# Performance work log

Measured on AMD Instinct MI355X. Metric: run time of the kernel, lower is better.

## Reference

```python
import jax, jax.numpy as jnp
import numpy as np

F_IN, U, N_CLS = 256, 512, 50


def _gru_scan(x_tbf, W, Uk, b):
    """Keras GRU (reset_after=True, tanh/sigmoid). x_tbf: [T,B,F]. Returns [T,B,U]."""
    b_in, b_rec = b[0], b[1]                 # each [3U]
    xg = jnp.einsum('tbf,fg->tbg', x_tbf, W) + b_in   # precompute input gates [T,B,3U]
    B = x_tbf.shape[1]
    h0 = jnp.zeros((B, U), dtype=x_tbf.dtype)

    def step(h, xt):
        rec = h @ Uk + b_rec                 # [B,3U]
        xz, xr, xh = jnp.split(xt, 3, axis=-1)
        rz, rr, rh = jnp.split(rec, 3, axis=-1)
        z = jax.nn.sigmoid(xz + rz)
        r = jax.nn.sigmoid(xr + rr)
        hh = jnp.tanh(xh + r * rh)
        h_new = z * h + (1.0 - z) * hh
        return h_new, h_new

    _, ys = jax.lax.scan(step, h0, xg)
    return ys


def setup_inputs() -> dict:
    key = jax.random.key(0)
    ks = jax.random.split(key, 10)
    x = jax.random.normal(ks[0], (32, 1024, F_IN), dtype=jnp.float32)
    # glorot-ish scales
    s_w = (2.0 / (F_IN + 3 * U)) ** 0.5
    s_u = (2.0 / (U + 3 * U)) ** 0.5
    s_d = (2.0 / (2 * U + N_CLS)) ** 0.5
    Wf = jax.random.normal(ks[1], (F_IN, 3 * U), dtype=jnp.float32) * s_w
    Uf = jax.random.normal(ks[2], (U, 3 * U), dtype=jnp.float32) * s_u
    bf = jnp.zeros((2, 3 * U), dtype=jnp.float32)
    Wb = jax.random.normal(ks[3], (F_IN, 3 * U), dtype=jnp.float32) * s_w
    Ub = jax.random.normal(ks[4], (U, 3 * U), dtype=jnp.float32) * s_u
    bb = jnp.zeros((2, 3 * U), dtype=jnp.float32)
    Wd = jax.random.normal(ks[5], (2 * U, N_CLS), dtype=jnp.float32) * s_d
    bd = jnp.zeros((N_CLS,), dtype=jnp.float32)
    return {"x": x, "Wf": Wf, "Uf": Uf, "bf": bf, "Wb": Wb, "Ub": Ub, "bb": bb, "Wd": Wd, "bd": bd}


def reference(x, Wf, Uf, bf, Wb, Ub, bb, Wd, bd):
    # training=False -> dropout / recurrent_dropout are identity.
    x_tbf = jnp.transpose(x, (1, 0, 2))                       # [T,B,F]
    fwd = _gru_scan(x_tbf, Wf, Uf, bf)                        # [T,B,U]
    bwd = _gru_scan(x_tbf[::-1], Wb, Ub, bb)[::-1]            # reversed-in, re-reversed out
    h = jnp.concatenate([fwd, bwd], axis=-1)                  # [T,B,2U]
    h = jnp.transpose(h, (1, 0, 2))                           # [B,T,2U]
    logits = jnp.einsum('btd,dc->btc', h, Wd) + bd            # [B,T,50]
    return jax.nn.softmax(logits, axis=-1)
```

## Files before the change

kernel.cpp:

```cpp
#include <hip/hip_runtime.h>
#include <hip/hip_bf16.h>

#define F_IN  256
#define UNITS 512
#define T_SEQ 1024
#define B_SZ  32
#define NCLS  50
#define NG    16
#define NWAVE 6
#define NTAGS 96
#define SCOPE __HIP_MEMORY_SCOPE_AGENT

typedef short s16x8 __attribute__((ext_vector_type(8)));
typedef float f32x16 __attribute__((ext_vector_type(16)));

__device__ __forceinline__ ushort f2bf(float f) {
  union { float f; unsigned u; } v; v.f = f;
  unsigned r = v.u + 0x7fffu + ((v.u >> 16) & 1u);
  return (ushort)(r >> 16);
}


__global__ void prep_xT(const float* __restrict__ x, ushort* __restrict__ xT) {
  int idx = blockIdx.x * 256 + threadIdx.x;
  int b = idx >> 15;
  int r = idx & 32767;
  int t = r >> 5;
  int c = r & 31;
  const float4* s4 = (const float4*)(x + ((size_t)b * T_SEQ + t) * F_IN + c * 8);
  float4 f0 = s4[0], f1 = s4[1];
  s16x8 o;
  o[0] = (short)f2bf(f0.x); o[1] = (short)f2bf(f0.y);
  o[2] = (short)f2bf(f0.z); o[3] = (short)f2bf(f0.w);
  o[4] = (short)f2bf(f1.x); o[5] = (short)f2bf(f1.y);
  o[6] = (short)f2bf(f1.z); o[7] = (short)f2bf(f1.w);
  *(s16x8*)(xT + ((size_t)t * B_SZ + b) * F_IN + c * 8) = o;
}

__global__ void prep_UWT(const float* __restrict__ Uf, const float* __restrict__ Wf,
                         const float* __restrict__ Ub, const float* __restrict__ Wb,
                         ushort* __restrict__ UWT) {
  int idx = blockIdx.x * 256 + threadIdx.x;
  int d = idx / 147456;
  int r = idx % 147456;
  int n = r / 96;
  int ck = r % 96;
  const float* U = d ? Ub : Uf;
  const float* W = d ? Wb : Wf;
  s16x8 o;
  #pragma unroll
  for (int i = 0; i < 8; ++i) {
    int k = ck * 8 + i;
    float v = (k < UNITS) ? U[(size_t)k * 1536 + n] : W[(size_t)(k - UNITS) * 1536 + n];
    o[i] = (short)f2bf(v);
  }
  *(s16x8*)(UWT + ((size_t)d * 1536 + n) * 768 + ck * 8) = o;
}

__global__ void prep_WdT(const float* __restrict__ Wd, ushort* __restrict__ WdT) {
  int idx = blockIdx.x * 256 + threadIdx.x;
  int n = idx >> 10, k = idx & 1023;
  float v = (n < NCLS) ? Wd[(size_t)k * NCLS + n] : 0.f;
  WdT[idx] = f2bf(v);
}

__global__ __launch_bounds__(384, 2) void gru_rec(
    const ushort* __restrict__ xT,
    const ushort* __restrict__ UWT,
    const float* __restrict__ bias_f,
    const float* __restrict__ bias_b,
    ushort* __restrict__ h_out,
    unsigned* __restrict__ tags)
{
  const int g  = blockIdx.x;
  const int d  = g >> 4;
  const int gg = g & 15;
  const int tid  = threadIdx.x;
  const int wv   = tid >> 6;
  const int lane = tid & 63;
  const int col  = lane & 31;
  const int half = lane >> 5;
  const int gate = wv >> 1;
  const int kh   = wv & 1;

  __shared__ float slot[2][32][128];

  s16x8 bfrag[24];
  {
    const ushort* bp = UWT + ((size_t)d * 1536 + gate * UNITS + gg * 32 + col) * 768
                       + kh * 384 + half * 8;
    #pragma unroll
    for (int c = 0; c < 24; ++c) bfrag[c] = *(const s16x8*)(bp + c * 16);
  }

  const float* bias = d ? bias_b : bias_f;
  float bz[3], br[3], bih[3], brh[3], hprev[3];
  #pragma unroll
  for (int i = 0; i < 3; ++i) {
    int e = tid + 384 * i;
    int j = gg * 32 + (e & 31);
    bz[i] = br[i] = bih[i] = brh[i] = 0.f;
    hprev[i] = 0.f;
    if (e < 1024) {
      bz[i]  = bias[j]        + bias[1536 + j];
      br[i]  = bias[512 + j]  + bias[1536 + 512 + j];
      bih[i] = bias[1024 + j];
      brh[i] = bias[1536 + 1024 + j];
    }
  }

  for (int s = 0; s < T_SEQ; ++s) {
    const int t_in = d ? (T_SEQ - 1 - s) : s;
    f32x16 acc_a, acc_b;
    #pragma unroll
    for (int i = 0; i < 16; ++i) { acc_a[i] = 0.f; acc_b[i] = 0.f; }

    if (kh) {
      const ushort* xp = xT + ((size_t)t_in * B_SZ + col) * F_IN + half * 8;
      #pragma unroll
      for (int grp = 0; grp < 2; ++grp) {
        s16x8 a[8];
        #pragma unroll
        for (int i = 0; i < 8; ++i) a[i] = *(const s16x8*)(xp + (grp * 8 + i) * 16);
        #pragma unroll
        for (int i = 0; i < 8; ++i)
          acc_b = __builtin_amdgcn_mfma_f32_32x32x16_bf16(a[i], bfrag[8 + grp * 8 + i], acc_b, 0, 0, 0);
      }
    }

    if (s > 0) {
      const unsigned expv = (unsigned)s;
      const unsigned* tg = tags + (size_t)(d * T_SEQ + (s - 1)) * NTAGS;
      bool ok;
      do {
        unsigned v0 = __hip_atomic_load(tg + lane, __ATOMIC_RELAXED, SCOPE);
        unsigned v1 = (lane < 32)
            ? __hip_atomic_load(tg + 64 + lane, __ATOMIC_RELAXED, SCOPE) : expv;
        ok = (v0 == expv) && (v1 == expv);
      } while (!__all(ok));
      __builtin_amdgcn_sched_barrier(0);
      asm volatile("" ::: "memory");

      const int t_prev = d ? (T_SEQ - s) : (s - 1);
      const ushort* ap = h_out + ((size_t)(d * T_SEQ + t_prev) * B_SZ + col) * UNITS
                         + kh * 384 + half * 8;
      if (kh) {
        s16x8 a[8];
        #pragma unroll
        for (int i = 0; i < 8; ++i) a[i] = *(const s16x8*)(ap + i * 16);
        #pragma unroll
        for (int i = 0; i < 8; ++i)
          acc_a = __builtin_amdgcn_mfma_f32_32x32x16_bf16(a[i], bfrag[i], acc_a, 0, 0, 0);
      } else {
        #pragma unroll
        for (int grp = 0; grp < 3; ++grp) {
          s16x8 a[8];
          #pragma unroll
          for (int i = 0; i < 8; ++i) a[i] = *(const s16x8*)(ap + (grp * 8 + i) * 16);
          #pragma unroll
          for (int i = 0; i < 8; ++i)
            acc_a = __builtin_amdgcn_mfma_f32_32x32x16_bf16(a[i], bfrag[grp * 8 + i], acc_a, 0, 0, 0);
        }
      }
    }

    #pragma unroll
    for (int i = 0; i < 16; ++i) {
      int brow = (i & 3) + 8 * (i >> 2) + 4 * half;
      if (gate < 2) {
        slot[kh][brow][gate * 32 + col] = acc_a[i] + acc_b[i];
      } else {
        slot[kh][brow][64 + col] = acc_a[i];
        if (kh) slot[1][brow][96 + col] = acc_b[i];
      }
    }
    __syncthreads();

    #pragma unroll
    for (int i = 0; i < 3; ++i) {
      int e = tid + 384 * i;
      if (e < 1024) {
        int b = e >> 5, j = e & 31;
        float rz = slot[0][b][j]      + slot[1][b][j]      + bz[i];
        float rr = slot[0][b][32 + j] + slot[1][b][32 + j] + br[i];
        float rh = slot[0][b][64 + j] + slot[1][b][64 + j] + brh[i];
        float xh = slot[1][b][96 + j] + bih[i];
        rz = fminf(fmaxf(rz, -30.f), 30.f);
        rr = fminf(fmaxf(rr, -30.f), 30.f);
        float z  = 1.f / (1.f + __expf(-rz));
        float rg = 1.f / (1.f + __expf(-rr));
        float ti = xh + rg * rh;
        ti = fminf(fmaxf(ti, -15.f), 15.f);
        float ex = __expf(2.f * ti);
        float hh = (ex - 1.f) / (ex + 1.f);
        float hn = z * hprev[i] + (1.f - z) * hh;
        hprev[i] = hn;
        __hip_atomic_store(
            h_out + ((size_t)(d * T_SEQ + t_in) * B_SZ + b) * UNITS + gg * 32 + j,
            (ushort)f2bf(hn), __ATOMIC_RELAXED, SCOPE);
      }
    }
    asm volatile("s_waitcnt vmcnt(0)" ::: "memory");
    if (lane == 0)
      __hip_atomic_store(tags + (size_t)(d * T_SEQ + s) * NTAGS + gg * NWAVE + wv,
                         (unsigned)(s + 1), __ATOMIC_RELAXED, SCOPE);
  }
}

__global__ __launch_bounds__(256) void dense_softmax(
    const ushort* __restrict__ h_out,
    const ushort* __restrict__ WdT,
    const float* __restrict__ bd,
    float* __restrict__ out)
{
  const int tid  = threadIdx.x;
  const int w    = tid >> 6, lane = tid & 63;
  const int col  = lane & 31, half = lane >> 5;
  const int t = blockIdx.x * 4 + w;

  __shared__ float lds[4][32][66];

  f32x16 acc0, acc1;
  #pragma unroll
  for (int i = 0; i < 16; ++i) { acc0[i] = 0.f; acc1[i] = 0.f; }

  const ushort* af  = h_out + ((size_t)t * B_SZ + col) * UNITS + half * 8;
  const ushort* ab  = h_out + ((size_t)(T_SEQ + t) * B_SZ + col) * UNITS + half * 8;
  const ushort* bp0 = WdT + (size_t)col * 1024 + half * 8;
  const ushort* bp1 = WdT + (size_t)(col + 32) * 1024 + half * 8;

  #pragma unroll 4
  for (int ks = 0; ks < 64; ++ks) {
    s16x8 a  = (ks < 32) ? *(const s16x8*)(af + ks * 16)
                         : *(const s16x8*)(ab + (ks - 32) * 16);
    s16x8 b0 = *(const s16x8*)(bp0 + ks * 16);
    s16x8 b1 = *(const s16x8*)(bp1 + ks * 16);
    acc0 = __builtin_amdgcn_mfma_f32_32x32x16_bf16(a, b0, acc0, 0, 0, 0);
    acc1 = __builtin_amdgcn_mfma_f32_32x32x16_bf16(a, b1, acc1, 0, 0, 0);
  }

  #pragma unroll
  for (int i = 0; i < 16; ++i) {
    int b = (i & 3) + 8 * (i >> 2) + 4 * half;
    lds[w][b][col]      = acc0[i];
    lds[w][b][32 + col] = acc1[i];
  }
  __syncthreads();

  if (tid < 128) {
    int tl = tid >> 5, b = tid & 31;
    int tt = blockIdx.x * 4 + tl;
    float v[NCLS];
    float m = -1e30f;
    #pragma unroll
    for (int c = 0; c < NCLS; ++c) { v[c] = lds[tl][b][c] + bd[c]; m = fmaxf(m, v[c]); }
    float sum = 0.f;
    #pragma unroll
    for (int c = 0; c < NCLS; ++c) { float e = __expf(v[c] - m); v[c] = e; sum += e; }
    float inv = 1.f / sum;
    float* op = out + ((size_t)b * T_SEQ + tt) * NCLS;
    #pragma unroll
    for (int c = 0; c < NCLS; ++c) op[c] = v[c] * inv;
  }
}

extern "C" void kernel_launch(void* const* d_in, const int* in_sizes, int n_in,
                              void* d_out, int out_size, void* d_ws, size_t ws_size,
                              hipStream_t stream) {
  const float* x  = (const float*)d_in[0];
  const float* Wf = (const float*)d_in[1];
  const float* Uf = (const float*)d_in[2];
  const float* bf = (const float*)d_in[3];
  const float* Wb = (const float*)d_in[4];
  const float* Ub = (const float*)d_in[5];
  const float* bb = (const float*)d_in[6];
  const float* Wd = (const float*)d_in[7];
  const float* bd = (const float*)d_in[8];
  float* out = (float*)d_out;

  char* ws = (char*)d_ws;
  ushort*   xT    = (ushort*)  (ws + 0);
  ushort*   UWT   = (ushort*)  (ws + 16777216);
  ushort*   WdTp  = (ushort*)  (ws + 21495808);
  ushort*   h_buf = (ushort*)  (ws + 21626880);
  unsigned* tags  = (unsigned*)(ws + 88735744);

  hipMemsetAsync(tags, 0, 2 * T_SEQ * NTAGS * sizeof(unsigned), stream);
  hipLaunchKernelGGL(prep_xT,       dim3(4096), dim3(256), 0, stream, x, xT);
  hipLaunchKernelGGL(prep_UWT,      dim3(1152), dim3(256), 0, stream, Uf, Wf, Ub, Wb, UWT);
  hipLaunchKernelGGL(prep_WdT,      dim3(256),  dim3(256), 0, stream, Wd, WdTp);
  hipLaunchKernelGGL(gru_rec,       dim3(32),   dim3(384), 0, stream, xT, UWT, bf, bb, h_buf, tags);
  hipLaunchKernelGGL(dense_softmax, dim3(256),  dim3(256), 0, stream, h_buf, WdTp, bd, out);
}
```

Baseline: 7.425 ms.

## Replace per-wave per-step tags with per-block monotonic step counters

Cross-block step synchronisation in the recurrent GRU kernel now uses one monotonic counter per workgroup per direction instead of a fresh tag per wave per timestep. Only one wave polls the counters, sleeping between polls, and the workgroup then joins at a barrier. A barrier before the counter publish replaces the per-wave vmcnt wait. This cuts polling traffic and the number of flags each step has to check, and shrinks the memset. In exchange it adds two workgroup barriers per step and relies on the barrier to make the h stores visible before the relaxed flag store. The recurrent h loads are also regrouped into batches of 12 instead of 8.

```diff
diff --git a/kernel.cpp b/kernel.cpp
--- a/kernel.cpp
+++ b/kernel.cpp
@@ -8,7 +8,6 @@
 #define NCLS  50
 #define NG    16
 #define NWAVE 6
-#define NTAGS 96
 #define SCOPE __HIP_MEMORY_SCOPE_AGENT
 
 typedef short s16x8 __attribute__((ext_vector_type(8)));
@@ -129,17 +128,18 @@
     }
 
     if (s > 0) {
-      const unsigned expv = (unsigned)s;
-      const unsigned* tg = tags + (size_t)(d * T_SEQ + (s - 1)) * NTAGS;
-      bool ok;
-      do {
-        unsigned v0 = __hip_atomic_load(tg + lane, __ATOMIC_RELAXED, SCOPE);
-        unsigned v1 = (lane < 32)
-            ? __hip_atomic_load(tg + 64 + lane, __ATOMIC_RELAXED, SCOPE) : expv;
-        ok = (v0 == expv) && (v1 == expv);
-      } while (!__all(ok));
-      __builtin_amdgcn_sched_barrier(0);
-      asm volatile("" ::: "memory");
+      if (wv == 0) {
+        const unsigned expv = (unsigned)s;
+        const unsigned* tg = tags + d * NG;
+        bool done;
+        do {
+          unsigned v = (lane < NG)
+              ? __hip_atomic_load(tg + lane, __ATOMIC_RELAXED, SCOPE) : expv;
+          done = __all(v >= expv);
+          if (!done) __builtin_amdgcn_s_sleep(1);
+        } while (!done);
+      }
+      __syncthreads();
 
       const int t_prev = d ? (T_SEQ - s) : (s - 1);
       const ushort* ap = h_out + ((size_t)(d * T_SEQ + t_prev) * B_SZ + col) * UNITS
@@ -153,13 +153,13 @@
           acc_a = __builtin_amdgcn_mfma_f32_32x32x16_bf16(a[i], bfrag[i], acc_a, 0, 0, 0);
       } else {
         #pragma unroll
-        for (int grp = 0; grp < 3; ++grp) {
-          s16x8 a[8];
+        for (int grp = 0; grp < 2; ++grp) {
+          s16x8 a[12];
           #pragma unroll
-          for (int i = 0; i < 8; ++i) a[i] = *(const s16x8*)(ap + (grp * 8 + i) * 16);
+          for (int i = 0; i < 12; ++i) a[i] = *(const s16x8*)(ap + (grp * 12 + i) * 16);
           #pragma unroll
-          for (int i = 0; i < 8; ++i)
-            acc_a = __builtin_amdgcn_mfma_f32_32x32x16_bf16(a[i], bfrag[grp * 8 + i], acc_a, 0, 0, 0);
+          for (int i = 0; i < 12; ++i)
+            acc_a = __builtin_amdgcn_mfma_f32_32x32x16_bf16(a[i], bfrag[grp * 12 + i], acc_a, 0, 0, 0);
         }
       }
     }
@@ -200,10 +200,10 @@
             (ushort)f2bf(hn), __ATOMIC_RELAXED, SCOPE);
       }
     }
-    asm volatile("s_waitcnt vmcnt(0)" ::: "memory");
-    if (lane == 0)
-      __hip_atomic_store(tags + (size_t)(d * T_SEQ + s) * NTAGS + gg * NWAVE + wv,
-                         (unsigned)(s + 1), __ATOMIC_RELAXED, SCOPE);
+    __syncthreads();
+    if (tid == 0)
+      __hip_atomic_store(tags + d * NG + gg, (unsigned)(s + 1),
+                         __ATOMIC_RELAXED, SCOPE);
   }
 }
 
@@ -285,7 +285,7 @@
   ushort*   h_buf = (ushort*)  (ws + 21626880);
   unsigned* tags  = (unsigned*)(ws + 88735744);
 
-  hipMemsetAsync(tags, 0, 2 * T_SEQ * NTAGS * sizeof(unsigned), stream);
+  hipMemsetAsync(tags, 0, 2 * NG * sizeof(unsigned), stream);
   hipLaunchKernelGGL(prep_xT,       dim3(4096), dim3(256), 0, stream, x, xT);
   hipLaunchKernelGGL(prep_UWT,      dim3(1152), dim3(256), 0, stream, Uf, Wf, Ub, Wb, UWT);
   hipLaunchKernelGGL(prep_WdT,      dim3(256),  dim3(256), 0, stream, Wd, WdTp);
```

New measurement: 7.077 ms. 4.7% less time.

## Replace per-step tag barrier with self-validating tagged hidden-state ring buffer

Applied to the files above, without the earlier changes.

The inter-block handshake changes. Each hidden value is now stored as a 32-bit word that packs the bf16 state with a 16-bit step counter, written into a double-buffered ring. Consumers poll the data words directly until every counter matches, which removes the separate tag write, the vmcnt(0) drain before it, and the extra round trip to read the tag before the data. The change also splits the MFMA accumulations into two independent chains and double-buffers the LDS slot by step parity. The cost is twice the bytes per recurrent load, heavier polling on wide data, and a 16-bit counter that relies on T_SEQ staying small.

```diff
diff --git a/kernel.cpp b/kernel.cpp
--- a/kernel.cpp
+++ b/kernel.cpp
@@ -7,8 +7,6 @@
 #define B_SZ  32
 #define NCLS  50
 #define NG    16
-#define NWAVE 6
-#define NTAGS 96
 #define SCOPE __HIP_MEMORY_SCOPE_AGENT
 
 typedef short s16x8 __attribute__((ext_vector_type(8)));
@@ -70,7 +68,7 @@
     const float* __restrict__ bias_f,
     const float* __restrict__ bias_b,
     ushort* __restrict__ h_out,
-    unsigned* __restrict__ tags)
+    unsigned* __restrict__ ring)
 {
   const int g  = blockIdx.x;
   const int d  = g >> 4;
@@ -83,7 +81,7 @@
   const int gate = wv >> 1;
   const int kh   = wv & 1;
 
-  __shared__ float slot[2][32][128];
+  __shared__ float slot[2][2][32][128];
 
   s16x8 bfrag[24];
   {
@@ -111,55 +109,61 @@
 
   for (int s = 0; s < T_SEQ; ++s) {
     const int t_in = d ? (T_SEQ - 1 - s) : s;
-    f32x16 acc_a, acc_b;
-    #pragma unroll
-    for (int i = 0; i < 16; ++i) { acc_a[i] = 0.f; acc_b[i] = 0.f; }
+    const int sb   = s & 1;
+    f32x16 acc_a, acc_a2, acc_b, acc_b2;
+    #pragma unroll
+    for (int i = 0; i < 16; ++i) { acc_a[i] = 0.f; acc_a2[i] = 0.f; acc_b[i] = 0.f; acc_b2[i] = 0.f; }
 
     if (kh) {
       const ushort* xp = xT + ((size_t)t_in * B_SZ + col) * F_IN + half * 8;
+      s16x8 a[16];
       #pragma unroll
-      for (int grp = 0; grp < 2; ++grp) {
-        s16x8 a[8];
-        #pragma unroll
-        for (int i = 0; i < 8; ++i) a[i] = *(const s16x8*)(xp + (grp * 8 + i) * 16);
-        #pragma unroll
-        for (int i = 0; i < 8; ++i)
-          acc_b = __builtin_amdgcn_mfma_f32_32x32x16_bf16(a[i], bfrag[8 + grp * 8 + i], acc_b, 0, 0, 0);
+      for (int i = 0; i < 16; ++i) a[i] = *(const s16x8*)(xp + i * 16);
+      #pragma unroll
+      for (int i = 0; i < 8; ++i) {
+        acc_b  = __builtin_amdgcn_mfma_f32_32x32x16_bf16(a[2*i],   bfrag[8 + 2*i],   acc_b,  0, 0, 0);
+        acc_b2 = __builtin_amdgcn_mfma_f32_32x32x16_bf16(a[2*i+1], bfrag[8 + 2*i+1], acc_b2, 0, 0, 0);
       }
     }
 
     if (s > 0) {
       const unsigned expv = (unsigned)s;
-      const unsigned* tg = tags + (size_t)(d * T_SEQ + (s - 1)) * NTAGS;
-      bool ok;
-      do {
-        unsigned v0 = __hip_atomic_load(tg + lane, __ATOMIC_RELAXED, SCOPE);
-        unsigned v1 = (lane < 32)
-            ? __hip_atomic_load(tg + 64 + lane, __ATOMIC_RELAXED, SCOPE) : expv;
-        ok = (v0 == expv) && (v1 == expv);
-      } while (!__all(ok));
-      __builtin_amdgcn_sched_barrier(0);
-      asm volatile("" ::: "memory");
-
-      const int t_prev = d ? (T_SEQ - s) : (s - 1);
-      const ushort* ap = h_out + ((size_t)(d * T_SEQ + t_prev) * B_SZ + col) * UNITS
-                         + kh * 384 + half * 8;
-      if (kh) {
-        s16x8 a[8];
+      const int p = (s - 1) & 1;
+      const unsigned* base = ring + (((size_t)(d * 2 + p) * B_SZ + col) * UNITS)
+                             + kh * 384 + half * 8;
+      const int nb = kh ? 1 : 3;
+      #pragma unroll
+      for (int b8 = 0; b8 < 3; ++b8) {
+        if (b8 >= nb) break;
+        unsigned long long q[8][4];
+        bool ok;
+        do {
+          #pragma unroll
+          for (int c2 = 0; c2 < 8; ++c2) {
+            const unsigned long long* qp =
+                (const unsigned long long*)(base + (b8 * 8 + c2) * 16);
+            #pragma unroll
+            for (int k = 0; k < 4; ++k)
+              q[c2][k] = __hip_atomic_load(qp + k, __ATOMIC_RELAXED, SCOPE);
+          }
+          ok = true;
+          #pragma unroll
+          for (int c2 = 0; c2 < 8; ++c2)
+            #pragma unroll
+            for (int k = 0; k < 4; ++k)
+              ok = ok && (((unsigned)q[c2][k] & 0xffffu) == expv)
+                      && (((unsigned)(q[c2][k] >> 32) & 0xffffu) == expv);
+        } while (!__all(ok));
         #pragma unroll
-        for (int i = 0; i < 8; ++i) a[i] = *(const s16x8*)(ap + i * 16);
-        #pragma unroll
-        for (int i = 0; i < 8; ++i)
-          acc_a = __builtin_amdgcn_mfma_f32_32x32x16_bf16(a[i], bfrag[i], acc_a, 0, 0, 0);
-      } else {
-        #pragma unroll
-        for (int grp = 0; grp < 3; ++grp) {
-          s16x8 a[8];
+        for (int c2 = 0; c2 < 8; ++c2) {
+          union { unsigned u[4]; s16x8 v; } A;
           #pragma unroll
-          for (int i = 0; i < 8; ++i) a[i] = *(const s16x8*)(ap + (grp * 8 + i) * 16);
-          #pragma unroll
-          for (int i = 0; i < 8; ++i)
-            acc_a = __builtin_amdgcn_mfma_f32_32x32x16_bf16(a[i], bfrag[grp * 8 + i], acc_a, 0, 0, 0);
+          for (int k = 0; k < 4; ++k)
+            A.u[k] = (((unsigned)(q[c2][k] >> 16)) & 0xffffu)
+                   | ((unsigned)(q[c2][k] >> 48) << 16);
+          int c = b8 * 8 + c2;
+          if (c2 & 1) acc_a2 = __builtin_amdgcn_mfma_f32_32x32x16_bf16(A.v, bfrag[c], acc_a2, 0, 0, 0);
+          else        acc_a  = __builtin_amdgcn_mfma_f32_32x32x16_bf16(A.v, bfrag[c], acc_a,  0, 0, 0);
         }
       }
     }
@@ -167,11 +171,13 @@
     #pragma unroll
     for (int i = 0; i < 16; ++i) {
       int brow = (i & 3) + 8 * (i >> 2) + 4 * half;
+      float ra = acc_a[i] + acc_a2[i];
+      float rb = acc_b[i] + acc_b2[i];
       if (gate < 2) {
-        slot[kh][brow][gate * 32 + col] = acc_a[i] + acc_b[i];
+        slot[sb][kh][brow][gate * 32 + col] = ra + rb;
       } else {
-        slot[kh][brow][64 + col] = acc_a[i];
-        if (kh) slot[1][brow][96 + col] = acc_b[i];
+        slot[sb][kh][brow][64 + col] = ra;
+        if (kh) slot[sb][1][brow][96 + col] = rb;
       }
     }
     __syncthreads();
@@ -181,10 +187,10 @@
       int e = tid + 384 * i;
       if (e < 1024) {
         int b = e >> 5, j = e & 31;
-        float rz = slot[0][b][j]      + slot[1][b][j]      + bz[i];
-        float rr = slot[0][b][32 + j] + slot[1][b][32 + j] + br[i];
-        float rh = slot[0][b][64 + j] + slot[1][b][64 + j] + brh[i];
-        float xh = slot[1][b][96 + j] + bih[i];
+        float rz = slot[sb][0][b][j]      + slot[sb][1][b][j]      + bz[i];
+        float rr = slot[sb][0][b][32 + j] + slot[sb][1][b][32 + j] + br[i];
+        float rh = slot[sb][0][b][64 + j] + slot[sb][1][b][64 + j] + brh[i];
+        float xh = slot[sb][1][b][96 + j] + bih[i];
         rz = fminf(fmaxf(rz, -30.f), 30.f);
         rr = fminf(fmaxf(rr, -30.f), 30.f);
         float z  = 1.f / (1.f + __expf(-rz));
@@ -195,23 +201,20 @@
         float hh = (ex - 1.f) / (ex + 1.f);
         float hn = z * hprev[i] + (1.f - z) * hh;
         hprev[i] = hn;
+        ushort hv = f2bf(hn);
+        unsigned w = ((unsigned)hv << 16) | (unsigned)(s + 1);
         __hip_atomic_store(
-            h_out + ((size_t)(d * T_SEQ + t_in) * B_SZ + b) * UNITS + gg * 32 + j,
-            (ushort)f2bf(hn), __ATOMIC_RELAXED, SCOPE);
-      }
-    }
-    asm volatile("s_waitcnt vmcnt(0)" ::: "memory");
-    if (lane == 0)
-      __hip_atomic_store(tags + (size_t)(d * T_SEQ + s) * NTAGS + gg * NWAVE + wv,
-                         (unsigned)(s + 1), __ATOMIC_RELAXED, SCOPE);
+            ring + (((size_t)(d * 2 + sb) * B_SZ + b) * UNITS) + gg * 32 + j,
+            w, __ATOMIC_RELAXED, SCOPE);
+        h_out[((size_t)(d * T_SEQ + t_in) * B_SZ + b) * UNITS + gg * 32 + j] = hv;
+      }
+    }
   }
 }
 
 __global__ __launch_bounds__(256) void dense_softmax(
-    const ushort* __restrict__ h_out,
-    const ushort* __restrict__ WdT,
-    const float* __restrict__ bd,
-    float* __restrict__ out)
+    const ushort* __restrict__ h_out, const ushort* __restrict__ WdT,
+    const float* __restrict__ bd, float* __restrict__ out)
 {
   const int tid  = threadIdx.x;
   const int w    = tid >> 6, lane = tid & 63;
@@ -283,12 +286,12 @@
   ushort*   UWT   = (ushort*)  (ws + 16777216);
   ushort*   WdTp  = (ushort*)  (ws + 21495808);
   ushort*   h_buf = (ushort*)  (ws + 21626880);
-  unsigned* tags  = (unsigned*)(ws + 88735744);
-
-  hipMemsetAsync(tags, 0, 2 * T_SEQ * NTAGS * sizeof(unsigned), stream);
+  unsigned* ring  = (unsigned*)(ws + 88735744);
+
+  hipMemsetAsync(ring, 0, 2 * 2 * B_SZ * UNITS * sizeof(unsigned), stream);
   hipLaunchKernelGGL(prep_xT,       dim3(4096), dim3(256), 0, stream, x, xT);
   hipLaunchKernelGGL(prep_UWT,      dim3(1152), dim3(256), 0, stream, Uf, Wf, Ub, Wb, UWT);
   hipLaunchKernelGGL(prep_WdT,      dim3(256),  dim3(256), 0, stream, Wd, WdTp);
-  hipLaunchKernelGGL(gru_rec,       dim3(32),   dim3(384), 0, stream, xT, UWT, bf, bb, h_buf, tags);
+  hipLaunchKernelGGL(gru_rec,       dim3(32),   dim3(384), 0, stream, xT, UWT, bf, bb, h_buf, ring);
   hipLaunchKernelGGL(dense_softmax, dim3(256),  dim3(256), 0, stream, h_buf, WdTp, bd, out);
 }
```

Result: slower. 18.03 ms (+142.9%).
